# Performance work log

Measured on AMD Instinct MI355X. Metric: run time of the kernel, lower is better.

The kernel has to match this reference:

```python
import jax, jax.numpy as jnp
import numpy as np

N_NODES = 100000
N_EDGES = 1600000
D = 64
N_GRAPHS = 64


def setup_inputs() -> dict:
    key = jax.random.key(0)
    ks = jax.random.split(key, 8)
    x = jax.random.normal(ks[0], (N_NODES, D), dtype=jnp.float32)
    edge_index = jax.random.randint(ks[1], (2, N_EDGES), 0, N_NODES)
    batch = jnp.sort(jax.random.randint(ks[2], (N_NODES,), 0, N_GRAPHS))
    edge_weight = jax.random.uniform(ks[3], (N_EDGES,), dtype=jnp.float32)
    s = 1.0 / np.sqrt(D)
    W1 = jax.random.normal(ks[4], (D, D), dtype=jnp.float32) * s
    b1 = jnp.zeros((D,), dtype=jnp.float32)
    W2 = jax.random.normal(ks[5], (D, D), dtype=jnp.float32) * s
    b2 = jnp.zeros((D,), dtype=jnp.float32)
    return {"x": x, "edge_index": edge_index, "batch": batch,
            "edge_weight": edge_weight, "W1": W1, "b1": b1, "W2": W2, "b2": b2}


def reference(x, edge_index, batch, edge_weight, W1, b1, W2, b2):
    # --- GCN normalization with self-loops (PyG gcn_norm, fill_value=1) ---
    loop = jnp.arange(N_NODES)
    src = jnp.concatenate([edge_index[0], loop])
    dst = jnp.concatenate([edge_index[1], loop])
    ew = jnp.concatenate([edge_weight, jnp.ones((N_NODES,), x.dtype)])
    deg = jax.ops.segment_sum(ew, dst, num_segments=N_NODES)
    dinv = jnp.where(deg > 0, jax.lax.rsqrt(deg), 0.0)
    norm = dinv[src] * ew * dinv[dst]  # [E+N]

    def gcn_relu(h, W, b):
        h = h @ W                                   # [N, D]
        msg = h[src] * norm[:, None]                # gather + weight messages
        agg = jax.ops.segment_sum(msg, dst, num_segments=N_NODES)
        return jax.nn.relu(agg + b)

    h = gcn_relu(x, W1, b1)
    h = gcn_relu(h, W2, b2)

    # --- global mean pool over graphs ---
    sums = jax.ops.segment_sum(h, batch, num_segments=N_GRAPHS)
    counts = jax.ops.segment_sum(jnp.ones((N_NODES, 1), h.dtype), batch,
                                 num_segments=N_GRAPHS)
    return sums / jnp.maximum(counts, 1.0)
```

## Files before the change

### kernel.cpp

```cpp
#include <hip/hip_runtime.h>

#define N_NODES 100000
#define N_EDGES 1600000
#define D 64
#define N_GRAPHS 64
#define NBLK ((N_NODES + 255) / 256)
#define WTS 68

__global__ void k_count_deg(const int* __restrict__ dst, const float* __restrict__ ew,
                            float* __restrict__ deg, int* __restrict__ cnt) {
    int e = blockIdx.x * blockDim.x + threadIdx.x;
    if (e < N_EDGES) {
        int d = dst[e];
        atomicAdd(&deg[d], ew[e]);
        atomicAdd(&cnt[d], 1);
    }
}

__global__ void k_scan1(const int* __restrict__ cnt, int* __restrict__ partial,
                        int* __restrict__ bsums, float* __restrict__ deg) {
    int t = threadIdx.x, b = blockIdx.x, i = b * 256 + t;
    if (i < N_NODES) {
        float d = deg[i];
        deg[i] = rsqrtf(d + 1.0f);
    }
    int v = (i < N_NODES) ? cnt[i] : 0;
    int incl = v;
    int lane = t & 63;
#pragma unroll
    for (int off = 1; off < 64; off <<= 1) {
        int u = __shfl_up(incl, off);
        if (lane >= off) incl += u;
    }
    __shared__ int wsum[4];
    int w = t >> 6;
    if (lane == 63) wsum[w] = incl;
    __syncthreads();
    int add = 0;
    for (int k = 0; k < w; ++k) add += wsum[k];
    incl += add;
    if (i < N_NODES) partial[i] = incl;
    if (t == 255) bsums[b] = incl;
}

__global__ void k_scan2(int* __restrict__ bsums) {
    __shared__ int s[512];
    int t = threadIdx.x;
    s[t] = (t < NBLK) ? bsums[t] : 0;
    __syncthreads();
    for (int off = 1; off < 512; off <<= 1) {
        int u = (t >= off) ? s[t - off] : 0;
        __syncthreads();
        s[t] += u;
        __syncthreads();
    }
    if (t < NBLK) bsums[t] = (t == 0) ? 0 : s[t - 1];
}

__global__ void k_scan3(const int* __restrict__ partial, const int* __restrict__ cnt,
                        const int* __restrict__ bsums, int* __restrict__ rowptr,
                        int* __restrict__ cursor) {
    int i = blockIdx.x * 256 + threadIdx.x;
    if (i < N_NODES) {
        int excl = partial[i] - cnt[i] + bsums[blockIdx.x];
        rowptr[i] = excl;
        cursor[i] = excl;
    }
}

__global__ void k_scatter(const int* __restrict__ src, const int* __restrict__ dst,
                          const float* __restrict__ ew, const float* __restrict__ dinv,
                          int* __restrict__ cursor, float2* __restrict__ csr) {
    int e = blockIdx.x * blockDim.x + threadIdx.x;
    if (e < N_EDGES) {
        int s = src[e];
        int d = dst[e];
        float nrm = dinv[s] * ew[e] * dinv[d];
        int pos = atomicAdd(&cursor[d], 1);
        csr[pos] = make_float2(__int_as_float(s), nrm);
    }
}

template <int LAYER>
__global__ __launch_bounds__(256) void k_layer(
        const float* __restrict__ in, const float* __restrict__ W,
        const float* __restrict__ bias, const float* __restrict__ dinv,
        const int* __restrict__ rowptr, const int* __restrict__ cnt,
        const float2* __restrict__ csr, const int* __restrict__ batch,
        float* __restrict__ outp) {
    __shared__ float WTs[D * WTS];
    __shared__ float aw[4][D];
    __shared__ float bs[D];

    {
        int t = threadIdx.x;
#pragma unroll
        for (int i = 0; i < 16; ++i) {
            int idx = t + i * 256;
            int k = idx >> 6, c = idx & 63;
            WTs[c * WTS + k] = W[idx];
        }
        if (t < D) bs[t] = bias[t];
    }
    __syncthreads();

    const int lane = threadIdx.x & 63;
    const int wid  = threadIdx.x >> 6;
    const int slot = lane >> 4;
    const int q    = lane & 15;
    float* awm = aw[wid];
    const float bl = bs[lane];
    const float4* in4 = (const float4*)in;

    int gw = (blockIdx.x * blockDim.x + threadIdx.x) >> 6;
    const int tw = (gridDim.x * blockDim.x) >> 6;

    for (int row = gw; row < N_NODES; row += tw) {
        const int st = __builtin_amdgcn_readfirstlane(rowptr[row]);
        const int dg = __builtin_amdgcn_readfirstlane(cnt[row]);
        const int dgm1 = dg - 1;

        float4 acc = make_float4(0.f, 0.f, 0.f, 0.f);
        {
            float di = dinv[row];
            if (slot == 0) {
                float4 s4 = in4[row * 16 + q];
                float d2 = di * di;
                acc.x = s4.x * d2; acc.y = s4.y * d2;
                acc.z = s4.z * d2; acc.w = s4.w * d2;
            }
        }

        for (int j = 0; j < dg; j += 16) {
            int ie = j + q;
            float2 c = csr[st + (ie < dgm1 ? ie : dgm1)];
            float sx0 = __shfl(c.x, 4 * 0 + slot);
            float wv0 = __shfl(c.y, 4 * 0 + slot);
            float sx1 = __shfl(c.x, 4 * 1 + slot);
            float wv1 = __shfl(c.y, 4 * 1 + slot);
            float sx2 = __shfl(c.x, 4 * 2 + slot);
            float wv2 = __shfl(c.y, 4 * 2 + slot);
            float sx3 = __shfl(c.x, 4 * 3 + slot);
            float wv3 = __shfl(c.y, 4 * 3 + slot);
            wv0 = (j + 0 + slot  < dg) ? wv0 : 0.f;
            wv1 = (j + 4 + slot  < dg) ? wv1 : 0.f;
            wv2 = (j + 8 + slot  < dg) ? wv2 : 0.f;
            wv3 = (j + 12 + slot < dg) ? wv3 : 0.f;
            int i0 = __float_as_int(sx0);
            int i1 = __float_as_int(sx1);
            int i2 = __float_as_int(sx2);
            int i3 = __float_as_int(sx3);
            float4 v0 = in4[i0 * 16 + q];
            float4 v1 = in4[i1 * 16 + q];
            float4 v2 = in4[i2 * 16 + q];
            float4 v3 = in4[i3 * 16 + q];
            acc.x = fmaf(v0.x, wv0, acc.x); acc.y = fmaf(v0.y, wv0, acc.y);
            acc.z = fmaf(v0.z, wv0, acc.z); acc.w = fmaf(v0.w, wv0, acc.w);
            acc.x = fmaf(v1.x, wv1, acc.x); acc.y = fmaf(v1.y, wv1, acc.y);
            acc.z = fmaf(v1.z, wv1, acc.z); acc.w = fmaf(v1.w, wv1, acc.w);
            acc.x = fmaf(v2.x, wv2, acc.x); acc.y = fmaf(v2.y, wv2, acc.y);
            acc.z = fmaf(v2.z, wv2, acc.z); acc.w = fmaf(v2.w, wv2, acc.w);
            acc.x = fmaf(v3.x, wv3, acc.x); acc.y = fmaf(v3.y, wv3, acc.y);
            acc.z = fmaf(v3.z, wv3, acc.z); acc.w = fmaf(v3.w, wv3, acc.w);
        }

        acc.x += __shfl_xor(acc.x, 16); acc.y += __shfl_xor(acc.y, 16);
        acc.z += __shfl_xor(acc.z, 16); acc.w += __shfl_xor(acc.w, 16);
        acc.x += __shfl_xor(acc.x, 32); acc.y += __shfl_xor(acc.y, 32);
        acc.z += __shfl_xor(acc.z, 32); acc.w += __shfl_xor(acc.w, 32);
        if (slot == 0) *(float4*)&awm[q * 4] = acc;

        float r0 = 0.f, r1 = 0.f, r2 = 0.f, r3 = 0.f;
#pragma unroll
        for (int t = 0; t < 16; ++t) {
            float4 a = *(const float4*)&awm[t * 4];
            float4 w = *(const float4*)&WTs[lane * WTS + t * 4];
            r0 = fmaf(a.x, w.x, r0);
            r1 = fmaf(a.y, w.y, r1);
            r2 = fmaf(a.z, w.z, r2);
            r3 = fmaf(a.w, w.w, r3);
        }
        float r = fmaxf((r0 + r1) + (r2 + r3) + bl, 0.f);

        if (LAYER == 1) {
            outp[row * D + lane] = r;
        } else {
            atomicAdd(&outp[batch[row] * D + lane], r);
        }
    }
}

__global__ void k_finalize(float* __restrict__ out, const int* __restrict__ batch) {
    int g = blockIdx.x;
    int lane = threadIdx.x;
    int lo = 0, hi = N_NODES;
    while (lo < hi) { int m = (lo + hi) >> 1; if (batch[m] < g) lo = m + 1; else hi = m; }
    int start = lo;
    hi = N_NODES;
    while (lo < hi) { int m = (lo + hi) >> 1; if (batch[m] < g + 1) lo = m + 1; else hi = m; }
    float c = (float)(lo - start);
    out[g * D + lane] /= fmaxf(c, 1.0f);
}

extern "C" void kernel_launch(void* const* d_in, const int* in_sizes, int n_in,
                              void* d_out, int out_size, void* d_ws, size_t ws_size,
                              hipStream_t stream) {
    const float* x     = (const float*)d_in[0];
    const int*   ei    = (const int*)d_in[1];
    const int*   src   = ei;
    const int*   dst   = ei + N_EDGES;
    const int*   batch = (const int*)d_in[2];
    const float* ew    = (const float*)d_in[3];
    const float* W1    = (const float*)d_in[4];
    const float* b1    = (const float*)d_in[5];
    const float* W2    = (const float*)d_in[6];
    const float* b2    = (const float*)d_in[7];
    float* out = (float*)d_out;

    char* ws = (char*)d_ws;
    float*  bufA   = (float*)(ws);
    float2* csr    = (float2*)(ws + 25600000);
    float*  deg    = (float*)(ws + 38400000);
    int*    cnt    = (int*)(ws + 38800000);
    int*    rowptr = (int*)(ws + 39200000);
    int*    cursor = (int*)(ws + 39600000);
    int*    bsums  = (int*)(ws + 40000000);

    hipMemsetAsync(deg, 0, N_NODES * sizeof(float), stream);
    hipMemsetAsync(cnt, 0, N_NODES * sizeof(int), stream);
    hipMemsetAsync(out, 0, N_GRAPHS * D * sizeof(float), stream);

    k_count_deg<<<(N_EDGES + 255) / 256, 256, 0, stream>>>(dst, ew, deg, cnt);
    k_scan1<<<NBLK, 256, 0, stream>>>(cnt, rowptr, bsums, deg);
    k_scan2<<<1, 512, 0, stream>>>(bsums);
    k_scan3<<<NBLK, 256, 0, stream>>>(rowptr, cnt, bsums, rowptr, cursor);
    k_scatter<<<(N_EDGES + 255) / 256, 256, 0, stream>>>(src, dst, ew, deg, cursor, csr);

    k_layer<1><<<2048, 256, 0, stream>>>(x, W1, b1, deg, rowptr, cnt, csr, batch, bufA);
    k_layer<2><<<2048, 256, 0, stream>>>(bufA, W2, b2, deg, rowptr, cnt, csr, batch, out);
    k_finalize<<<N_GRAPHS, D, 0, stream>>>(out, batch);
}
```

Measured before the change: 508.1 us.

## Split aggregation into fp16 column-sliced gather with XCC-affine work stealing

Converts node features and the hidden layer to fp16 stored as four 16-column slices, so each random-gather slice (about 3.2 MB) can stay resident in one XCD's L2. The aggregation becomes its own kernel that reads the hardware XCC id and starts on its own slice, taking 64-row chunks from an atomic queue per slice. The GEMM and ReLU move to a separate kernel. This cuts gather bytes and improves cache locality, at the cost of fp16 rounding, an extra fp32 agg round trip through memory, and more kernel launches.

```diff
diff --git a/kernel.cpp b/kernel.cpp
--- a/kernel.cpp
+++ b/kernel.cpp
@@ -1,4 +1,5 @@
 #include <hip/hip_runtime.h>
+#include <hip/hip_fp16.h>
 
 #define N_NODES 100000
 #define N_EDGES 1600000
@@ -6,6 +7,9 @@
 #define N_GRAPHS 64
 #define NBLK ((N_NODES + 255) / 256)
 #define WTS 68
+#define NS16 (N_NODES * 16)
+#define CH 64
+#define NCH ((N_NODES + CH - 1) / CH)
 
 __global__ void k_count_deg(const int* __restrict__ dst, const float* __restrict__ ew,
                             float* __restrict__ deg, int* __restrict__ cnt) {
@@ -81,17 +85,77 @@
     }
 }
 
-template <int LAYER>
-__global__ __launch_bounds__(256) void k_layer(
-        const float* __restrict__ in, const float* __restrict__ W,
-        const float* __restrict__ bias, const float* __restrict__ dinv,
-        const int* __restrict__ rowptr, const int* __restrict__ cnt,
-        const float2* __restrict__ csr, const int* __restrict__ batch,
-        float* __restrict__ outp) {
+__global__ void k_half(const float* __restrict__ x, __half* __restrict__ xs) {
+    int idx = blockIdx.x * blockDim.x + threadIdx.x;
+    const int total = N_NODES * D;
+    const int stride = gridDim.x * blockDim.x;
+    for (; idx < total; idx += stride) {
+        int node = idx >> 6, c = idx & 63;
+        xs[(size_t)(c >> 4) * NS16 + node * 16 + (c & 15)] = __float2half_rn(x[idx]);
+    }
+}
+
+__global__ __launch_bounds__(256) void k_agg(
+        const __half* __restrict__ tabs, const float2* __restrict__ csr,
+        const float* __restrict__ dinv, const int* __restrict__ rowptr,
+        const int* __restrict__ cnt, float* __restrict__ agg,
+        int* __restrict__ qcnt) {
+    __shared__ int shc;
+    int xcc;
+    asm volatile("s_getreg_b32 %0, hwreg(20, 0, 32)" : "=s"(xcc));
+    const int myslice = xcc & 3;
+    const int lane = threadIdx.x & 63;
+    const int wid  = threadIdx.x >> 6;
+    const int slot = lane >> 4;
+    const int f    = lane & 15;
+
+    for (int qi = 0; qi < 4; ++qi) {
+        const int q = (myslice + qi) & 3;
+        const __half* __restrict__ tab = tabs + (size_t)q * NS16;
+        for (;;) {
+            __syncthreads();
+            if (threadIdx.x == 0) shc = atomicAdd(&qcnt[q], 1);
+            __syncthreads();
+            const int ch = shc;
+            if (ch >= NCH) break;
+            const int rlo = ch * CH;
+            const int rhi = rlo + CH < N_NODES ? rlo + CH : N_NODES;
+            for (int row = rlo + wid; row < rhi; row += 4) {
+                int st = __builtin_amdgcn_readfirstlane(rowptr[row]);
+                int dg = __builtin_amdgcn_readfirstlane(cnt[row]);
+                float di = dinv[row];
+                float acc = (slot == 0)
+                    ? __half2float(tab[row * 16 + f]) * (di * di) : 0.f;
+                const int dgm1 = dg - 1;
+                for (int j = 0; j < dg; j += 8) {
+                    int e0 = j + slot, e1 = j + 4 + slot;
+                    float2 c0 = csr[st + (e0 < dgm1 ? e0 : dgm1)];
+                    float2 c1 = csr[st + (e1 < dgm1 ? e1 : dgm1)];
+                    float w0 = (e0 < dg) ? c0.y : 0.f;
+                    float w1 = (e1 < dg) ? c1.y : 0.f;
+                    int i0 = __float_as_int(c0.x);
+                    int i1 = __float_as_int(c1.x);
+                    float v0 = __half2float(tab[i0 * 16 + f]);
+                    float v1 = __half2float(tab[i1 * 16 + f]);
+                    acc = fmaf(v0, w0, acc);
+                    acc = fmaf(v1, w1, acc);
+                }
+                acc += __shfl_xor(acc, 16);
+                acc += __shfl_xor(acc, 32);
+                if (slot == 0) agg[(size_t)row * D + q * 16 + f] = acc;
+            }
+        }
+    }
+}
+
+template <int MODE>
+__global__ __launch_bounds__(256) void k_gemm(
+        const float* __restrict__ inrows, const float* __restrict__ W,
+        const float* __restrict__ bias, const int* __restrict__ batch,
+        __half* __restrict__ outh, float* __restrict__ outf) {
     __shared__ float WTs[D * WTS];
     __shared__ float aw[4][D];
     __shared__ float bs[D];
-
     {
         int t = threadIdx.x;
 #pragma unroll
@@ -106,70 +170,14 @@
 
     const int lane = threadIdx.x & 63;
     const int wid  = threadIdx.x >> 6;
-    const int slot = lane >> 4;
-    const int q    = lane & 15;
     float* awm = aw[wid];
     const float bl = bs[lane];
-    const float4* in4 = (const float4*)in;
 
     int gw = (blockIdx.x * blockDim.x + threadIdx.x) >> 6;
     const int tw = (gridDim.x * blockDim.x) >> 6;
 
     for (int row = gw; row < N_NODES; row += tw) {
-        const int st = __builtin_amdgcn_readfirstlane(rowptr[row]);
-        const int dg = __builtin_amdgcn_readfirstlane(cnt[row]);
-        const int dgm1 = dg - 1;
-
-        float4 acc = make_float4(0.f, 0.f, 0.f, 0.f);
-        {
-            float di = dinv[row];
-            if (slot == 0) {
-                float4 s4 = in4[row * 16 + q];
-                float d2 = di * di;
-                acc.x = s4.x * d2; acc.y = s4.y * d2;
-                acc.z = s4.z * d2; acc.w = s4.w * d2;
-            }
-        }
-
-        for (int j = 0; j < dg; j += 16) {
-            int ie = j + q;
-            float2 c = csr[st + (ie < dgm1 ? ie : dgm1)];
-            float sx0 = __shfl(c.x, 4 * 0 + slot);
-            float wv0 = __shfl(c.y, 4 * 0 + slot);
-            float sx1 = __shfl(c.x, 4 * 1 + slot);
-            float wv1 = __shfl(c.y, 4 * 1 + slot);
-            float sx2 = __shfl(c.x, 4 * 2 + slot);
-            float wv2 = __shfl(c.y, 4 * 2 + slot);
-            float sx3 = __shfl(c.x, 4 * 3 + slot);
-            float wv3 = __shfl(c.y, 4 * 3 + slot);
-            wv0 = (j + 0 + slot  < dg) ? wv0 : 0.f;
-            wv1 = (j + 4 + slot  < dg) ? wv1 : 0.f;
-            wv2 = (j + 8 + slot  < dg) ? wv2 : 0.f;
-            wv3 = (j + 12 + slot < dg) ? wv3 : 0.f;
-            int i0 = __float_as_int(sx0);
-            int i1 = __float_as_int(sx1);
-            int i2 = __float_as_int(sx2);
-            int i3 = __float_as_int(sx3);
-            float4 v0 = in4[i0 * 16 + q];
-            float4 v1 = in4[i1 * 16 + q];
-            float4 v2 = in4[i2 * 16 + q];
-            float4 v3 = in4[i3 * 16 + q];
-            acc.x = fmaf(v0.x, wv0, acc.x); acc.y = fmaf(v0.y, wv0, acc.y);
-            acc.z = fmaf(v0.z, wv0, acc.z); acc.w = fmaf(v0.w, wv0, acc.w);
-            acc.x = fmaf(v1.x, wv1, acc.x); acc.y = fmaf(v1.y, wv1, acc.y);
-            acc.z = fmaf(v1.z, wv1, acc.z); acc.w = fmaf(v1.w, wv1, acc.w);
-            acc.x = fmaf(v2.x, wv2, acc.x); acc.y = fmaf(v2.y, wv2, acc.y);
-            acc.z = fmaf(v2.z, wv2, acc.z); acc.w = fmaf(v2.w, wv2, acc.w);
-            acc.x = fmaf(v3.x, wv3, acc.x); acc.y = fmaf(v3.y, wv3, acc.y);
-            acc.z = fmaf(v3.z, wv3, acc.z); acc.w = fmaf(v3.w, wv3, acc.w);
-        }
-
-        acc.x += __shfl_xor(acc.x, 16); acc.y += __shfl_xor(acc.y, 16);
-        acc.z += __shfl_xor(acc.z, 16); acc.w += __shfl_xor(acc.w, 16);
-        acc.x += __shfl_xor(acc.x, 32); acc.y += __shfl_xor(acc.y, 32);
-        acc.z += __shfl_xor(acc.z, 32); acc.w += __shfl_xor(acc.w, 32);
-        if (slot == 0) *(float4*)&awm[q * 4] = acc;
-
+        awm[lane] = inrows[(size_t)row * D + lane];
         float r0 = 0.f, r1 = 0.f, r2 = 0.f, r3 = 0.f;
 #pragma unroll
         for (int t = 0; t < 16; ++t) {
@@ -181,11 +189,11 @@
             r3 = fmaf(a.w, w.w, r3);
         }
         float r = fmaxf((r0 + r1) + (r2 + r3) + bl, 0.f);
-
-        if (LAYER == 1) {
-            outp[row * D + lane] = r;
+        if (MODE == 0) {
+            outh[(size_t)(lane >> 4) * NS16 + row * 16 + (lane & 15)] =
+                __float2half_rn(r);
         } else {
-            atomicAdd(&outp[batch[row] * D + lane], r);
+            atomicAdd(&outf[batch[row] * D + lane], r);
         }
     }
 }
@@ -218,25 +226,32 @@
     float* out = (float*)d_out;
 
     char* ws = (char*)d_ws;
-    float*  bufA   = (float*)(ws);
-    float2* csr    = (float2*)(ws + 25600000);
-    float*  deg    = (float*)(ws + 38400000);
-    int*    cnt    = (int*)(ws + 38800000);
-    int*    rowptr = (int*)(ws + 39200000);
-    int*    cursor = (int*)(ws + 39600000);
-    int*    bsums  = (int*)(ws + 40000000);
+    __half* xsh    = (__half*)(ws);
+    __half* hh     = (__half*)(ws + 12800000);
+    float*  agg    = (float*)(ws + 25600000);
+    float2* csr    = (float2*)(ws + 51200000);
+    float*  deg    = (float*)(ws + 64000000);
+    int*    cnt    = (int*)(ws + 64400000);
+    int*    rowptr = (int*)(ws + 64800000);
+    int*    cursor = (int*)(ws + 65200000);
+    int*    bsums  = (int*)(ws + 65600000);
+    int*    qcnt   = (int*)(ws + 65604096);
 
     hipMemsetAsync(deg, 0, N_NODES * sizeof(float), stream);
     hipMemsetAsync(cnt, 0, N_NODES * sizeof(int), stream);
     hipMemsetAsync(out, 0, N_GRAPHS * D * sizeof(float), stream);
-
+    hipMemsetAsync(qcnt, 0, 8 * sizeof(int), stream);
+
+    k_half<<<1024, 256, 0, stream>>>(x, xsh);
     k_count_deg<<<(N_EDGES + 255) / 256, 256, 0, stream>>>(dst, ew, deg, cnt);
     k_scan1<<<NBLK, 256, 0, stream>>>(cnt, rowptr, bsums, deg);
     k_scan2<<<1, 512, 0, stream>>>(bsums);
     k_scan3<<<NBLK, 256, 0, stream>>>(rowptr, cnt, bsums, rowptr, cursor);
     k_scatter<<<(N_EDGES + 255) / 256, 256, 0, stream>>>(src, dst, ew, deg, cursor, csr);
 
-    k_layer<1><<<2048, 256, 0, stream>>>(x, W1, b1, deg, rowptr, cnt, csr, batch, bufA);
-    k_layer<2><<<2048, 256, 0, stream>>>(bufA, W2, b2, deg, rowptr, cnt, csr, batch, out);
+    k_agg<<<4096, 256, 0, stream>>>(xsh, csr, deg, rowptr, cnt, agg, qcnt);
+    k_gemm<0><<<2048, 256, 0, stream>>>(agg, W1, b1, batch, hh, out);
+    k_agg<<<4096, 256, 0, stream>>>(hh, csr, deg, rowptr, cnt, agg, qcnt + 4);
+    k_gemm<1><<<2048, 256, 0, stream>>>(agg, W2, b2, batch, hh, out);
     k_finalize<<<N_GRAPHS, D, 0, stream>>>(out, batch);
 }
```

Result: slower. 1.045 ms (+105.6%).
